# Kernel tuning notes

Measured on AMD Instinct MI355X. Metric: run time of the kernel, lower is better.

Reference implementation:

```python
import jax, jax.numpy as jnp
import numpy as np

N, F, H, CLS = 50000, 64, 128, 64   # nodes, node_features, second_features, num_classes
E, EL = 800000, 200000              # graph edges, decode (label) edges


def setup_inputs() -> dict:
    key = jax.random.key(0)
    ks = jax.random.split(key, 12)
    sc = lambda k, sh, fan: (jax.random.normal(k, sh, jnp.float32) / np.sqrt(fan)).astype(jnp.float32)
    return dict(
        x=jax.random.normal(ks[0], (N, F), jnp.float32),
        edge_index=jax.random.randint(ks[1], (2, E), 0, N),
        edge_label_index=jax.random.randint(ks[2], (2, EL), 0, N),
        hidden1=jnp.zeros((N, H), jnp.float32),   # H state of GCLSTM
        hidden2=jnp.zeros((N, H), jnp.float32),   # C state of GCLSTM
        # GCNConv params
        W_gcn=sc(ks[3], (F, F), F),
        b_gcn=jnp.zeros((F,), jnp.float32),
        # GCLSTM params, gates stacked along last axis in order (i, f, c, o)
        Wx=sc(ks[4], (F, 4 * H), F),      # input->gate weights W_i..W_o
        Th=sc(ks[5], (H, 4 * H), H),      # ChebConv(K=1) thetas on H (pure linear)
        b_gate=jnp.zeros((4 * H,), jnp.float32),  # b_i, b_f, b_c, b_o
        b_conv=jnp.zeros((4 * H,), jnp.float32),  # ChebConv biases
        w_c=sc(ks[6], (3, H), H),         # peephole w_c_i, w_c_f, w_c_o
        # output Linear
        W_lin=sc(ks[7], (H, CLS), H),
        b_lin=jnp.zeros((CLS,), jnp.float32),
    )


def _gcn(x, src, dst, W, b, n):
    """PyG GCNConv: add self-loops, symmetric D^-1/2 (A+I) D^-1/2 normalization."""
    xw = x @ W                                   # [N,F]
    loop = jnp.arange(n)
    src = jnp.concatenate([src, loop])
    dst = jnp.concatenate([dst, loop])
    deg = jax.ops.segment_sum(jnp.ones(src.shape, jnp.float32), dst, num_segments=n)
    dinv = jnp.where(deg > 0, jax.lax.rsqrt(deg), 0.0)
    norm = dinv[src] * dinv[dst]                 # [E+N]
    agg = jax.ops.segment_sum(norm[:, None] * xw[src], dst, num_segments=n)
    return agg + b


def reference(x, edge_index, edge_label_index, hidden1, hidden2,
              W_gcn, b_gcn, Wx, Th, b_gate, b_conv, w_c, W_lin, b_lin):
    n = x.shape[0]
    h = _gcn(x, edge_index[0], edge_index[1], W_gcn, b_gcn, n)   # GCNConv  [N,F]
    # GCLSTM, K=1: ChebConv on H degenerates to H @ Theta + b_conv
    g = (h @ Wx + b_gate) + (hidden1 @ Th + b_conv)              # [N,4H]
    gi, gf, gc, go = jnp.split(g, 4, axis=1)
    I = jax.nn.sigmoid(gi + w_c[0] * hidden2)
    Fg = jax.nn.sigmoid(gf + w_c[1] * hidden2)
    C = Fg * hidden2 + I * jnp.tanh(gc)
    O = jax.nn.sigmoid(go + w_c[2] * C)          # peephole on NEW cell state
    Hn = O * jnp.tanh(C)                         # [N,H]
    z = jax.nn.softmax(jax.nn.relu(Hn) @ W_lin + b_lin, axis=1)  # [N,CLS]
    # decode: dot product of endpoint embeddings
    r = jnp.sum(z[edge_label_index[0]] * z[edge_label_index[1]], axis=-1)  # [EL]
    # faithful to the original forward: returns input hidden1 and the NEW cell state
    return (r, hidden1, C)
```

## Files before the change

### kernel.cpp

```cpp
#include <hip/hip_runtime.h>
#include <math.h>

#define FDIM 64
#define HDIM 128
#define CLSD 64

#define NPART 8
#define MAXDEG 64

typedef unsigned short ushort_t;
typedef _Float16 hfrag __attribute__((ext_vector_type(8)));
typedef float f32x4 __attribute__((ext_vector_type(4)));

#define LOG2E 1.4426950408889634f

__device__ __forceinline__ float ex2(float x){ float r; asm("v_exp_f32 %0, %1" : "=v"(r) : "v"(x)); return r; }
__device__ __forceinline__ float rcp_(float x){ float r; asm("v_rcp_f32 %0, %1" : "=v"(r) : "v"(x)); return r; }
__device__ __forceinline__ float fsigmoid(float x){ return rcp_(1.0f + ex2(-LOG2E*x)); }
__device__ __forceinline__ float ftanh(float x){ return 1.0f - 2.0f*rcp_(1.0f + ex2(2.0f*LOG2E*x)); }

__device__ __forceinline__ ushort_t f2h(float f){
    _Float16 h = (_Float16)f;
    ushort_t u; __builtin_memcpy(&u, &h, 2); return u;
}
__device__ __forceinline__ float hflo(unsigned int u){
    ushort_t v = (ushort_t)u; _Float16 h; __builtin_memcpy(&h, &v, 2); return (float)h;
}
__device__ __forceinline__ float hfhi(unsigned int u){
    ushort_t v = (ushort_t)(u >> 16); _Float16 h; __builtin_memcpy(&h, &v, 2); return (float)h;
}
__device__ __forceinline__ unsigned int pk2h(float a, float b){
    return (unsigned int)f2h(a) | ((unsigned int)f2h(b) << 16);
}


__launch_bounds__(256)
__global__ void k_pre(const float* __restrict__ x,  const float* __restrict__ Wg,
                      const float* __restrict__ bg,
                      const float* __restrict__ Wx, const float* __restrict__ Th,
                      const float* __restrict__ Wl,
                      const float* __restrict__ bga, const float* __restrict__ bco,
                      const float* __restrict__ h1,
                      ushort_t* __restrict__ Bh, ushort_t* __restrict__ Lh,
                      float* __restrict__ bsum, int* __restrict__ cnt,
                      ushort_t* __restrict__ xh, ushort_t* __restrict__ Ab,
                      float* __restrict__ oh1, int N, int N2){
    int tid = blockIdx.x*256 + threadIdx.x;
    const int secW = 107008 + N;
    const int secX = secW + N*8;
    if (tid < 98304){
        int k = tid >> 9, col = tid & 511;
        float v;
        if (k < 64){
            float acc = 0.f;
            #pragma unroll 8
            for (int f = 0; f < 64; ++f) acc += Wg[k*64 + f]*Wx[f*512 + col];
            v = acc;
        } else {
            v = Th[(k-64)*512 + col];
        }
        int g = col >> 7, hc = col & 127;
        int w = hc >> 5, within = hc & 31;
        int c8 = g*2 + (within >> 4);
        int T = w*8 + c8;
        int s = k >> 5;
        int lane = ((k >> 3) & 3)*16 + (within & 15);
        int pos = ((T*6 + s)*64 + lane)*8 + (k & 7);
        Bh[pos] = f2h(v);
    } else if (tid < 106496){
        int i = tid - 98304;
        int k = i >> 6, col = i & 63;
        float v = Wl[k*64 + col];
        int ct = col >> 4;
        int s = k >> 5;
        int lane = ((k >> 3) & 3)*16 + (col & 15);
        int pos = ((ct*4 + s)*64 + lane)*8 + (k & 7);
        Lh[pos] = f2h(v);
    } else if (tid < 107008){
        int c = tid - 106496;
        float acc = bga[c] + bco[c];
        #pragma unroll 8
        for (int f = 0; f < 64; ++f) acc += bg[f]*Wx[f*512 + c];
        bsum[c] = acc;
    } else if (tid < secW){
        cnt[tid - 107008] = 0;
    } else if (tid < secX){
        int i = tid - secW;
        const float4* xp = (const float4*)(x + (size_t)i*8);
        float4 p0 = xp[0], p1 = xp[1];
        ((int4*)xh)[i] = make_int4((int)pk2h(p0.x,p0.y), (int)pk2h(p0.z,p0.w),
                                   (int)pk2h(p1.x,p1.y), (int)pk2h(p1.z,p1.w));
    } else {
        int i = tid - secX;
        if (i >= N2*16) return;
        int n = i >> 4, q = i & 15;
        int4 frag = make_int4(0,0,0,0);
        if (n < N){
            const float4* src = (const float4*)(h1 + (size_t)n*128 + q*8);
            float4 p0 = src[0], p1 = src[1];
            float4* dst = (float4*)(oh1 + (size_t)n*128 + q*8);
            dst[0] = p0; dst[1] = p1;
            frag = make_int4((int)pk2h(p0.x,p0.y), (int)pk2h(p0.z,p0.w),
                             (int)pk2h(p1.x,p1.y), (int)pk2h(p1.z,p1.w));
        }
        int s = 2 + (q >> 2);
        int lane = (q & 3)*16 + (n & 15);
        ((int4*)Ab)[((size_t)(n >> 4)*6 + s)*64 + lane] = frag;
    }
}

__launch_bounds__(256)
__global__ void k_fill(const int* __restrict__ ei, int* __restrict__ cnt,
                       int* __restrict__ ell, int E, int psz){
    int p   = blockIdx.x % NPART;
    int bi  = blockIdx.x / NPART;
    int bpp = gridDim.x / NPART;
    int chunk = (E + bpp - 1) / bpp;
    int beg = bi*chunk;
    int end = beg + chunk; if (end > E) end = E;
    int lo = p*psz, hi = lo + psz;
    for (int i = beg + threadIdx.x; i < end; i += 256){
        int d = ei[E + i];
        if (d >= lo && d < hi){
            int s = ei[i];
            int slot = atomicAdd(&cnt[d], 1);
            if (slot < MAXDEG) ell[(size_t)d*MAXDEG + slot] = s;
        }
    }
}

__launch_bounds__(256)
__global__ void k_dinv(const int* __restrict__ cnt, float* __restrict__ dinv, int N){
    int i = blockIdx.x*256 + threadIdx.x;
    if (i < N) dinv[i] = rsqrtf((float)cnt[i] + 1.0f);
}

__launch_bounds__(256)
__global__ void k_gather(const int* __restrict__ cnt, const int* __restrict__ ell,
                         const float* __restrict__ dinv, const ushort_t* __restrict__ xh,
                         ushort_t* __restrict__ Ab, int N, int N2){
    int tid = blockIdx.x*256 + threadIdx.x;
    int n = tid >> 3, q = tid & 7;
    if (n >= N2) return;
    int s_ = q >> 2;
    int lane = (q & 3)*16 + (n & 15);
    size_t fpos = ((size_t)(n >> 4)*6 + s_)*64 + lane;
    if (n >= N){
        ((int4*)Ab)[fpos] = make_int4(0,0,0,0);
        return;
    }
    int cn = cnt[n]; if (cn > MAXDEG) cn = MAXDEG;
    const int* row = ell + (size_t)n*MAXDEG;
    const int4* xv = (const int4*)xh;
    float a0=0.f,a1=0.f,a2=0.f,a3=0.f,a4=0.f,a5=0.f,a6=0.f,a7=0.f;
    int idx = 0;
    for (; idx + 4 <= cn; idx += 4){
        int s0 = row[idx], s1 = row[idx+1], s2 = row[idx+2], s3 = row[idx+3];
        float w0 = dinv[s0], w1 = dinv[s1], w2 = dinv[s2], w3 = dinv[s3];
        int4 u = xv[(size_t)s0*8 + q];
        int4 p = xv[(size_t)s1*8 + q];
        int4 v = xv[(size_t)s2*8 + q];
        int4 z = xv[(size_t)s3*8 + q];
        a0 += w0*hflo((unsigned)u.x) + w1*hflo((unsigned)p.x) + w2*hflo((unsigned)v.x) + w3*hflo((unsigned)z.x);
        a1 += w0*hfhi((unsigned)u.x) + w1*hfhi((unsigned)p.x) + w2*hfhi((unsigned)v.x) + w3*hfhi((unsigned)z.x);
        a2 += w0*hflo((unsigned)u.y) + w1*hflo((unsigned)p.y) + w2*hflo((unsigned)v.y) + w3*hflo((unsigned)z.y);
        a3 += w0*hfhi((unsigned)u.y) + w1*hfhi((unsigned)p.y) + w2*hfhi((unsigned)v.y) + w3*hfhi((unsigned)z.y);
        a4 += w0*hflo((unsigned)u.z) + w1*hflo((unsigned)p.z) + w2*hflo((unsigned)v.z) + w3*hflo((unsigned)z.z);
        a5 += w0*hfhi((unsigned)u.z) + w1*hfhi((unsigned)p.z) + w2*hfhi((unsigned)v.z) + w3*hfhi((unsigned)z.z);
        a6 += w0*hflo((unsigned)u.w) + w1*hflo((unsigned)p.w) + w2*hflo((unsigned)v.w) + w3*hflo((unsigned)z.w);
        a7 += w0*hfhi((unsigned)u.w) + w1*hfhi((unsigned)p.w) + w2*hfhi((unsigned)v.w) + w3*hfhi((unsigned)z.w);
    }
    for (; idx < cn; ++idx){
        int s0 = row[idx];
        float w0 = dinv[s0];
        int4 u = xv[(size_t)s0*8 + q];
        a0 += w0*hflo((unsigned)u.x); a1 += w0*hfhi((unsigned)u.x);
        a2 += w0*hflo((unsigned)u.y); a3 += w0*hfhi((unsigned)u.y);
        a4 += w0*hflo((unsigned)u.z); a5 += w0*hfhi((unsigned)u.z);
        a6 += w0*hflo((unsigned)u.w); a7 += w0*hfhi((unsigned)u.w);
    }
    float dn = dinv[n];
    int4 sv = xv[(size_t)n*8 + q];
    a0 = dn*(a0 + dn*hflo((unsigned)sv.x));
    a1 = dn*(a1 + dn*hfhi((unsigned)sv.x));
    a2 = dn*(a2 + dn*hflo((unsigned)sv.y));
    a3 = dn*(a3 + dn*hfhi((unsigned)sv.y));
    a4 = dn*(a4 + dn*hflo((unsigned)sv.z));
    a5 = dn*(a5 + dn*hfhi((unsigned)sv.z));
    a6 = dn*(a6 + dn*hflo((unsigned)sv.w));
    a7 = dn*(a7 + dn*hfhi((unsigned)sv.w));
    ((int4*)Ab)[fpos] = make_int4((int)pk2h(a0,a1), (int)pk2h(a2,a3),
                                  (int)pk2h(a4,a5), (int)pk2h(a6,a7));
}

__launch_bounds__(512)
__global__ void k_fused(const ushort_t* __restrict__ Ab, const float* __restrict__ h2,
                        const ushort_t* __restrict__ Bh, const ushort_t* __restrict__ Lh,
                        const float* __restrict__ bsum, const float* __restrict__ wc,
                        const float* __restrict__ blin,
                        float* __restrict__ outC, ushort_t* __restrict__ zb, int N)
{
    __shared__ __align__(16) char smem[33792];
    ushort_t* Hh   = (ushort_t*)smem;
    float*    Ltile = (float*)(smem + 16384);

    const int t    = threadIdx.x;
    const int w    = t >> 6;
    const int wm   = w >> 2;
    const int wn   = w & 3;
    const int lane = t & 63;
    const int nb   = blockIdx.x * 64;
    const size_t bt = (size_t)blockIdx.x * 4;

    f32x4 acc[2][8];
    #pragma unroll
    for (int mt = 0; mt < 2; ++mt)
        #pragma unroll
        for (int c8 = 0; c8 < 8; ++c8)
            acc[mt][c8] = (f32x4){0.f,0.f,0.f,0.f};

    const hfrag* AF  = (const hfrag*)Ab;
    const hfrag* BhF = (const hfrag*)Bh;

    #pragma unroll
    for (int s = 0; s < 6; ++s){
        hfrag a0 = AF[((bt + wm*2 + 0)*6 + s)*64 + lane];
        hfrag a1 = AF[((bt + wm*2 + 1)*6 + s)*64 + lane];
        #pragma unroll
        for (int c8 = 0; c8 < 8; ++c8){
            int T = wn*8 + c8;
            hfrag bh = BhF[(T*6 + s)*64 + lane];
            acc[0][c8] = __builtin_amdgcn_mfma_f32_16x16x32_f16(a0, bh, acc[0][c8], 0,0,0);
            acc[1][c8] = __builtin_amdgcn_mfma_f32_16x16x32_f16(a1, bh, acc[1][c8], 0,0,0);
        }
    }

    #pragma unroll
    for (int hc_t = 0; hc_t < 2; ++hc_t){
        int hc  = wn*32 + hc_t*16 + (lane & 15);
        float bi = bsum[hc],       bfv = bsum[128 + hc];
        float bc = bsum[256 + hc], bo  = bsum[384 + hc];
        float wci = wc[hc], wcf = wc[128 + hc], wco = wc[256 + hc];
        #pragma unroll
        for (int mt = 0; mt < 2; ++mt){
            #pragma unroll
            for (int rr = 0; rr < 4; ++rr){
                int row = wm*32 + mt*16 + ((lane >> 4) & 3)*4 + rr;
                int gr  = nb + row;
                float gi = acc[mt][0 + hc_t][rr] + bi;
                float gf = acc[mt][2 + hc_t][rr] + bfv;
                float gc = acc[mt][4 + hc_t][rr] + bc;
                float go = acc[mt][6 + hc_t][rr] + bo;
                float hv = (gr < N) ? h2[(size_t)gr*128 + hc] : 0.0f;
                float I  = fsigmoid(gi + wci*hv);
                float Fg = fsigmoid(gf + wcf*hv);
                float C  = Fg*hv + I*ftanh(gc);
                float O  = fsigmoid(go + wco*C);
                float hn = O*ftanh(C);
                if (gr < N) outC[(size_t)gr*128 + hc] = C;
                float hr = fmaxf(hn, 0.0f);
                int l2  = (row & 15) + (hc_t*2 + ((lane >> 3) & 1))*16;
                int pos = (((wm*2 + mt)*4 + wn)*64 + l2)*8 + (lane & 7);
                Hh[pos] = f2h(hr);
            }
        }
    }
    __syncthreads();

    const hfrag* HF  = (const hfrag*)Hh;
    const hfrag* LhF = (const hfrag*)Lh;
    f32x4 acc2[2];
    acc2[0] = (f32x4){0.f,0.f,0.f,0.f};
    acc2[1] = (f32x4){0.f,0.f,0.f,0.f};
    #pragma unroll
    for (int sp = 0; sp < 4; ++sp){
        hfrag a0 = HF[((wm*2+0)*4 + sp)*64 + lane];
        hfrag a1 = HF[((wm*2+1)*4 + sp)*64 + lane];
        hfrag bh = LhF[(wn*4 + sp)*64 + lane];
        acc2[0] = __builtin_amdgcn_mfma_f32_16x16x32_f16(a0, bh, acc2[0], 0,0,0);
        acc2[1] = __builtin_amdgcn_mfma_f32_16x16x32_f16(a1, bh, acc2[1], 0,0,0);
    }
    {
        int cls = wn*16 + (lane & 15);
        float bv = blin[cls];
        #pragma unroll
        for (int mtl = 0; mtl < 2; ++mtl){
            #pragma unroll
            for (int rr = 0; rr < 4; ++rr){
                int row = wm*32 + mtl*16 + ((lane >> 4) & 3)*4 + rr;
                Ltile[row*68 + cls] = acc2[mtl][rr] + bv;
            }
        }
    }
    __syncthreads();

    {
        int m = t >> 3, q = t & 7;
        const float4* Lr = (const float4*)&Ltile[m*68 + q*8];
        float4 v0 = Lr[0], v1 = Lr[1];
        float mx = fmaxf(fmaxf(fmaxf(v0.x,v0.y),fmaxf(v0.z,v0.w)),
                         fmaxf(fmaxf(v1.x,v1.y),fmaxf(v1.z,v1.w)));
        #pragma unroll
        for (int off2 = 1; off2 < 8; off2 <<= 1) mx = fmaxf(mx, __shfl_xor(mx, off2, 64));
        float e[8];
        e[0]=ex2(LOG2E*(v0.x-mx)); e[1]=ex2(LOG2E*(v0.y-mx));
        e[2]=ex2(LOG2E*(v0.z-mx)); e[3]=ex2(LOG2E*(v0.w-mx));
        e[4]=ex2(LOG2E*(v1.x-mx)); e[5]=ex2(LOG2E*(v1.y-mx));
        e[6]=ex2(LOG2E*(v1.z-mx)); e[7]=ex2(LOG2E*(v1.w-mx));
        float s8 = e[0]+e[1]+e[2]+e[3]+e[4]+e[5]+e[6]+e[7];
        #pragma unroll
        for (int off2 = 1; off2 < 8; off2 <<= 1) s8 += __shfl_xor(s8, off2, 64);
        float inv = rcp_(s8);
        if (nb + m < N){
            ((int4*)zb)[(size_t)(nb+m)*8 + q] =
                make_int4((int)pk2h(e[0]*inv, e[1]*inv), (int)pk2h(e[2]*inv, e[3]*inv),
                          (int)pk2h(e[4]*inv, e[5]*inv), (int)pk2h(e[6]*inv, e[7]*inv));
        }
    }
}

__launch_bounds__(256)
__global__ void k_dec(const int* __restrict__ eli, const ushort_t* __restrict__ zb,
                      float* __restrict__ r, int EL){
    int tid = blockIdx.x*256 + threadIdx.x;
    int e = tid >> 3, l = tid & 7;
    if (e >= EL) return;
    int s = eli[e], d = eli[EL + e];
    int4 a = ((const int4*)zb)[(size_t)s*8 + l];
    int4 b = ((const int4*)zb)[(size_t)d*8 + l];
    unsigned int ua[4] = {(unsigned)a.x,(unsigned)a.y,(unsigned)a.z,(unsigned)a.w};
    unsigned int ub[4] = {(unsigned)b.x,(unsigned)b.y,(unsigned)b.z,(unsigned)b.w};
    float p = 0.f;
    #pragma unroll
    for (int j = 0; j < 4; ++j){
        p += hflo(ua[j])*hflo(ub[j]) + hfhi(ua[j])*hfhi(ub[j]);
    }
    #pragma unroll
    for (int off = 1; off < 8; off <<= 1) p += __shfl_xor(p, off, 64);
    if (l == 0) r[e] = p;
}

extern "C" void kernel_launch(void* const* d_in, const int* in_sizes, int n_in,
                              void* d_out, int out_size, void* d_ws, size_t ws_size,
                              hipStream_t stream)
{
    const float* x   = (const float*)d_in[0];
    const int*   ei  = (const int*)  d_in[1];
    const int*   eli = (const int*)  d_in[2];
    const float* h1  = (const float*)d_in[3];
    const float* h2  = (const float*)d_in[4];
    const float* Wg  = (const float*)d_in[5];
    const float* bg  = (const float*)d_in[6];
    const float* Wx  = (const float*)d_in[7];
    const float* Th  = (const float*)d_in[8];
    const float* bga = (const float*)d_in[9];
    const float* bco = (const float*)d_in[10];
    const float* wc  = (const float*)d_in[11];
    const float* Wl  = (const float*)d_in[12];
    const float* bl  = (const float*)d_in[13];

    const int N  = in_sizes[0] / FDIM;
    const int E  = in_sizes[1] / 2;
    const int EL = in_sizes[2] / 2;
    const int N2 = (N + 63) & ~63;
    const int PSZ = (N + NPART - 1) / NPART;

    float* ws   = (float*)d_ws;
    ushort_t* xh = (ushort_t*)ws;
    ushort_t* Ab = xh + (size_t)N*64;
    ushort_t* zb = Ab + (size_t)N2*192;
    float* dinv = (float*)(zb + (size_t)N*64);
    int*   cnt  = (int*)(dinv + N);
    int*   ell  = cnt + N;
    size_t base = (size_t)((ell + (size_t)N*MAXDEG) - (int*)ws);
    base = (base + 3) & ~(size_t)3;
    ushort_t* Bh = (ushort_t*)(ws + base);
    ushort_t* Lh = Bh + 98304;
    float*  bsum = (float*)(Lh + 8192);

    float* out = (float*)d_out;
    float* r   = out;
    float* oh1 = out + EL;
    float* oC  = out + EL + (size_t)N*HDIM;

    const int preThreads = 107008 + N + N*8 + N2*16;
    const int epBlocks   = NPART * 256;
    k_pre   <<<(preThreads + 255)/256, 256, 0, stream>>>(x, Wg, bg, Wx, Th, Wl, bga, bco,
                                                         h1, Bh, Lh, bsum, cnt,
                                                         xh, Ab, oh1, N, N2);
    k_fill  <<<epBlocks, 256, 0, stream>>>(ei, cnt, ell, E, PSZ);
    k_dinv  <<<(N + 255)/256, 256, 0, stream>>>(cnt, dinv, N);
    k_gather<<<((size_t)N2*8 + 255)/256, 256, 0, stream>>>(cnt, ell, dinv, xh, Ab, N, N2);
    k_fused <<<N2/64, 512, 0, stream>>>(Ab, h2, Bh, Lh, bsum, wc, bl, oC, zb, N);
    k_dec   <<<(EL*8 + 255)/256, 256, 0, stream>>>(eli, zb, r, EL);
}
```

Baseline: 121.0 us.

## Merge edge fill into prep kernel, drop dinv pass, shrink fused tile

The edge-bucketing (ELL fill) is folded into the preprocessing kernel as extra blocks, and the degree counter is zeroed with an async memset. The separate dinv kernel is removed and gather computes rsqrt of the degree counts inline. The fused GEMM/LSTM/softmax kernel now uses 16-row tiles with 256 threads and less shared memory, giving more blocks for occupancy. The aim is fewer launches and better occupancy, at the cost of redundant rsqrt work and the B-weight fragments being reloaded by four times as many blocks.

```diff
diff --git a/kernel.cpp b/kernel.cpp
--- a/kernel.cpp
+++ b/kernel.cpp
@@ -40,14 +40,34 @@
                       const float* __restrict__ Wx, const float* __restrict__ Th,
                       const float* __restrict__ Wl,
                       const float* __restrict__ bga, const float* __restrict__ bco,
-                      const float* __restrict__ h1,
+                      const float* __restrict__ h1, const int* __restrict__ ei,
                       ushort_t* __restrict__ Bh, ushort_t* __restrict__ Lh,
                       float* __restrict__ bsum, int* __restrict__ cnt,
+                      int* __restrict__ ell,
                       ushort_t* __restrict__ xh, ushort_t* __restrict__ Ab,
-                      float* __restrict__ oh1, int N, int N2){
-    int tid = blockIdx.x*256 + threadIdx.x;
-    const int secW = 107008 + N;
-    const int secX = secW + N*8;
+                      float* __restrict__ oh1, int N, int N2, int E, int psz,
+                      int epBlocks){
+    int t = threadIdx.x;
+    if ((int)blockIdx.x < epBlocks){
+        int p   = blockIdx.x % NPART;
+        int bi  = blockIdx.x / NPART;
+        int bpp = epBlocks / NPART;
+        int chunk = (E + bpp - 1) / bpp;
+        int beg = bi*chunk;
+        int end = beg + chunk; if (end > E) end = E;
+        int lo = p*psz, hi = lo + psz;
+        for (int i = beg + t; i < end; i += 256){
+            int d = ei[E + i];
+            if (d >= lo && d < hi){
+                int s = ei[i];
+                int slot = atomicAdd(&cnt[d], 1);
+                if (slot < MAXDEG) ell[(size_t)d*MAXDEG + slot] = s;
+            }
+        }
+        return;
+    }
+    int tid = ((int)blockIdx.x - epBlocks)*256 + t;
+    const int secX = 107008 + N*8;
     if (tid < 98304){
         int k = tid >> 9, col = tid & 511;
         float v;
@@ -82,10 +102,8 @@
         #pragma unroll 8
         for (int f = 0; f < 64; ++f) acc += bg[f]*Wx[f*512 + c];
         bsum[c] = acc;
-    } else if (tid < secW){
-        cnt[tid - 107008] = 0;
     } else if (tid < secX){
-        int i = tid - secW;
+        int i = tid - 107008;
         const float4* xp = (const float4*)(x + (size_t)i*8);
         float4 p0 = xp[0], p1 = xp[1];
         ((int4*)xh)[i] = make_int4((int)pk2h(p0.x,p0.y), (int)pk2h(p0.z,p0.w),
@@ -110,34 +128,8 @@
 }
 
 __launch_bounds__(256)
-__global__ void k_fill(const int* __restrict__ ei, int* __restrict__ cnt,
-                       int* __restrict__ ell, int E, int psz){
-    int p   = blockIdx.x % NPART;
-    int bi  = blockIdx.x / NPART;
-    int bpp = gridDim.x / NPART;
-    int chunk = (E + bpp - 1) / bpp;
-    int beg = bi*chunk;
-    int end = beg + chunk; if (end > E) end = E;
-    int lo = p*psz, hi = lo + psz;
-    for (int i = beg + threadIdx.x; i < end; i += 256){
-        int d = ei[E + i];
-        if (d >= lo && d < hi){
-            int s = ei[i];
-            int slot = atomicAdd(&cnt[d], 1);
-            if (slot < MAXDEG) ell[(size_t)d*MAXDEG + slot] = s;
-        }
-    }
-}
-
-__launch_bounds__(256)
-__global__ void k_dinv(const int* __restrict__ cnt, float* __restrict__ dinv, int N){
-    int i = blockIdx.x*256 + threadIdx.x;
-    if (i < N) dinv[i] = rsqrtf((float)cnt[i] + 1.0f);
-}
-
-__launch_bounds__(256)
 __global__ void k_gather(const int* __restrict__ cnt, const int* __restrict__ ell,
-                         const float* __restrict__ dinv, const ushort_t* __restrict__ xh,
+                         const ushort_t* __restrict__ xh,
                          ushort_t* __restrict__ Ab, int N, int N2){
     int tid = blockIdx.x*256 + threadIdx.x;
     int n = tid >> 3, q = tid & 7;
@@ -156,7 +148,10 @@
     int idx = 0;
     for (; idx + 4 <= cn; idx += 4){
         int s0 = row[idx], s1 = row[idx+1], s2 = row[idx+2], s3 = row[idx+3];
-        float w0 = dinv[s0], w1 = dinv[s1], w2 = dinv[s2], w3 = dinv[s3];
+        float w0 = rsqrtf((float)cnt[s0] + 1.0f);
+        float w1 = rsqrtf((float)cnt[s1] + 1.0f);
+        float w2 = rsqrtf((float)cnt[s2] + 1.0f);
+        float w3 = rsqrtf((float)cnt[s3] + 1.0f);
         int4 u = xv[(size_t)s0*8 + q];
         int4 p = xv[(size_t)s1*8 + q];
         int4 v = xv[(size_t)s2*8 + q];
@@ -172,14 +167,14 @@
     }
     for (; idx < cn; ++idx){
         int s0 = row[idx];
-        float w0 = dinv[s0];
+        float w0 = rsqrtf((float)cnt[s0] + 1.0f);
         int4 u = xv[(size_t)s0*8 + q];
         a0 += w0*hflo((unsigned)u.x); a1 += w0*hfhi((unsigned)u.x);
         a2 += w0*hflo((unsigned)u.y); a3 += w0*hfhi((unsigned)u.y);
         a4 += w0*hflo((unsigned)u.z); a5 += w0*hfhi((unsigned)u.z);
         a6 += w0*hflo((unsigned)u.w); a7 += w0*hfhi((unsigned)u.w);
     }
-    float dn = dinv[n];
+    float dn = rsqrtf((float)cn + 1.0f);
     int4 sv = xv[(size_t)n*8 + q];
     a0 = dn*(a0 + dn*hflo((unsigned)sv.x));
     a1 = dn*(a1 + dn*hfhi((unsigned)sv.x));
@@ -193,128 +188,104 @@
                                   (int)pk2h(a4,a5), (int)pk2h(a6,a7));
 }
 
-__launch_bounds__(512)
+__launch_bounds__(256)
 __global__ void k_fused(const ushort_t* __restrict__ Ab, const float* __restrict__ h2,
                         const ushort_t* __restrict__ Bh, const ushort_t* __restrict__ Lh,
                         const float* __restrict__ bsum, const float* __restrict__ wc,
                         const float* __restrict__ blin,
                         float* __restrict__ outC, ushort_t* __restrict__ zb, int N)
 {
-    __shared__ __align__(16) char smem[33792];
+    __shared__ __align__(16) char smem[8448];
     ushort_t* Hh   = (ushort_t*)smem;
-    float*    Ltile = (float*)(smem + 16384);
+    float*    Ltile = (float*)(smem + 4096);
 
     const int t    = threadIdx.x;
     const int w    = t >> 6;
-    const int wm   = w >> 2;
-    const int wn   = w & 3;
     const int lane = t & 63;
-    const int nb   = blockIdx.x * 64;
-    const size_t bt = (size_t)blockIdx.x * 4;
-
-    f32x4 acc[2][8];
-    #pragma unroll
-    for (int mt = 0; mt < 2; ++mt)
-        #pragma unroll
-        for (int c8 = 0; c8 < 8; ++c8)
-            acc[mt][c8] = (f32x4){0.f,0.f,0.f,0.f};
+    const int nb   = blockIdx.x * 16;
+
+    f32x4 acc[8];
+    #pragma unroll
+    for (int c8 = 0; c8 < 8; ++c8) acc[c8] = (f32x4){0.f,0.f,0.f,0.f};
 
     const hfrag* AF  = (const hfrag*)Ab;
     const hfrag* BhF = (const hfrag*)Bh;
 
     #pragma unroll
     for (int s = 0; s < 6; ++s){
-        hfrag a0 = AF[((bt + wm*2 + 0)*6 + s)*64 + lane];
-        hfrag a1 = AF[((bt + wm*2 + 1)*6 + s)*64 + lane];
+        hfrag a0 = AF[((size_t)blockIdx.x*6 + s)*64 + lane];
         #pragma unroll
         for (int c8 = 0; c8 < 8; ++c8){
-            int T = wn*8 + c8;
+            int T = w*8 + c8;
             hfrag bh = BhF[(T*6 + s)*64 + lane];
-            acc[0][c8] = __builtin_amdgcn_mfma_f32_16x16x32_f16(a0, bh, acc[0][c8], 0,0,0);
-            acc[1][c8] = __builtin_amdgcn_mfma_f32_16x16x32_f16(a1, bh, acc[1][c8], 0,0,0);
+            acc[c8] = __builtin_amdgcn_mfma_f32_16x16x32_f16(a0, bh, acc[c8], 0,0,0);
         }
     }
 
     #pragma unroll
     for (int hc_t = 0; hc_t < 2; ++hc_t){
-        int hc  = wn*32 + hc_t*16 + (lane & 15);
+        int hc  = w*32 + hc_t*16 + (lane & 15);
         float bi = bsum[hc],       bfv = bsum[128 + hc];
         float bc = bsum[256 + hc], bo  = bsum[384 + hc];
         float wci = wc[hc], wcf = wc[128 + hc], wco = wc[256 + hc];
         #pragma unroll
-        for (int mt = 0; mt < 2; ++mt){
-            #pragma unroll
-            for (int rr = 0; rr < 4; ++rr){
-                int row = wm*32 + mt*16 + ((lane >> 4) & 3)*4 + rr;
-                int gr  = nb + row;
-                float gi = acc[mt][0 + hc_t][rr] + bi;
-                float gf = acc[mt][2 + hc_t][rr] + bfv;
-                float gc = acc[mt][4 + hc_t][rr] + bc;
-                float go = acc[mt][6 + hc_t][rr] + bo;
-                float hv = (gr < N) ? h2[(size_t)gr*128 + hc] : 0.0f;
-                float I  = fsigmoid(gi + wci*hv);
-                float Fg = fsigmoid(gf + wcf*hv);
-                float C  = Fg*hv + I*ftanh(gc);
-                float O  = fsigmoid(go + wco*C);
-                float hn = O*ftanh(C);
-                if (gr < N) outC[(size_t)gr*128 + hc] = C;
-                float hr = fmaxf(hn, 0.0f);
-                int l2  = (row & 15) + (hc_t*2 + ((lane >> 3) & 1))*16;
-                int pos = (((wm*2 + mt)*4 + wn)*64 + l2)*8 + (lane & 7);
-                Hh[pos] = f2h(hr);
-            }
+        for (int rr = 0; rr < 4; ++rr){
+            int row = ((lane >> 4) & 3)*4 + rr;
+            int gr  = nb + row;
+            float gi = acc[0 + hc_t][rr] + bi;
+            float gf = acc[2 + hc_t][rr] + bfv;
+            float gc = acc[4 + hc_t][rr] + bc;
+            float go = acc[6 + hc_t][rr] + bo;
+            float hv = (gr < N) ? h2[(size_t)gr*128 + hc] : 0.0f;
+            float I  = fsigmoid(gi + wci*hv);
+            float Fg = fsigmoid(gf + wcf*hv);
+            float C  = Fg*hv + I*ftanh(gc);
+            float O  = fsigmoid(go + wco*C);
+            float hn = O*ftanh(C);
+            if (gr < N) outC[(size_t)gr*128 + hc] = C;
+            float hr = fmaxf(hn, 0.0f);
+            int l2  = row + (hc_t*2 + ((lane >> 3) & 1))*16;
+            int pos = (w*64 + l2)*8 + (lane & 7);
+            Hh[pos] = f2h(hr);
         }
     }
     __syncthreads();
 
     const hfrag* HF  = (const hfrag*)Hh;
     const hfrag* LhF = (const hfrag*)Lh;
-    f32x4 acc2[2];
-    acc2[0] = (f32x4){0.f,0.f,0.f,0.f};
-    acc2[1] = (f32x4){0.f,0.f,0.f,0.f};
+    f32x4 acc2 = (f32x4){0.f,0.f,0.f,0.f};
     #pragma unroll
     for (int sp = 0; sp < 4; ++sp){
-        hfrag a0 = HF[((wm*2+0)*4 + sp)*64 + lane];
-        hfrag a1 = HF[((wm*2+1)*4 + sp)*64 + lane];
-        hfrag bh = LhF[(wn*4 + sp)*64 + lane];
-        acc2[0] = __builtin_amdgcn_mfma_f32_16x16x32_f16(a0, bh, acc2[0], 0,0,0);
-        acc2[1] = __builtin_amdgcn_mfma_f32_16x16x32_f16(a1, bh, acc2[1], 0,0,0);
+        hfrag a0 = HF[sp*64 + lane];
+        hfrag bh = LhF[(w*4 + sp)*64 + lane];
+        acc2 = __builtin_amdgcn_mfma_f32_16x16x32_f16(a0, bh, acc2, 0,0,0);
     }
     {
-        int cls = wn*16 + (lane & 15);
+        int cls = w*16 + (lane & 15);
         float bv = blin[cls];
         #pragma unroll
-        for (int mtl = 0; mtl < 2; ++mtl){
-            #pragma unroll
-            for (int rr = 0; rr < 4; ++rr){
-                int row = wm*32 + mtl*16 + ((lane >> 4) & 3)*4 + rr;
-                Ltile[row*68 + cls] = acc2[mtl][rr] + bv;
-            }
+        for (int rr = 0; rr < 4; ++rr){
+            int row = ((lane >> 4) & 3)*4 + rr;
+            Ltile[row*68 + cls] = acc2[rr] + bv;
         }
     }
     __syncthreads();
 
     {
-        int m = t >> 3, q = t & 7;
-        const float4* Lr = (const float4*)&Ltile[m*68 + q*8];
-        float4 v0 = Lr[0], v1 = Lr[1];
-        float mx = fmaxf(fmaxf(fmaxf(v0.x,v0.y),fmaxf(v0.z,v0.w)),
-                         fmaxf(fmaxf(v1.x,v1.y),fmaxf(v1.z,v1.w)));
-        #pragma unroll
-        for (int off2 = 1; off2 < 8; off2 <<= 1) mx = fmaxf(mx, __shfl_xor(mx, off2, 64));
-        float e[8];
-        e[0]=ex2(LOG2E*(v0.x-mx)); e[1]=ex2(LOG2E*(v0.y-mx));
-        e[2]=ex2(LOG2E*(v0.z-mx)); e[3]=ex2(LOG2E*(v0.w-mx));
-        e[4]=ex2(LOG2E*(v1.x-mx)); e[5]=ex2(LOG2E*(v1.y-mx));
-        e[6]=ex2(LOG2E*(v1.z-mx)); e[7]=ex2(LOG2E*(v1.w-mx));
-        float s8 = e[0]+e[1]+e[2]+e[3]+e[4]+e[5]+e[6]+e[7];
-        #pragma unroll
-        for (int off2 = 1; off2 < 8; off2 <<= 1) s8 += __shfl_xor(s8, off2, 64);
-        float inv = rcp_(s8);
+        int m = t >> 4, q4 = t & 15;
+        float4 v0 = *(const float4*)&Ltile[m*68 + q4*4];
+        float mx = fmaxf(fmaxf(v0.x,v0.y), fmaxf(v0.z,v0.w));
+        #pragma unroll
+        for (int off2 = 1; off2 < 16; off2 <<= 1) mx = fmaxf(mx, __shfl_xor(mx, off2, 64));
+        float e0 = ex2(LOG2E*(v0.x-mx)), e1 = ex2(LOG2E*(v0.y-mx));
+        float e2 = ex2(LOG2E*(v0.z-mx)), e3 = ex2(LOG2E*(v0.w-mx));
+        float s4 = e0+e1+e2+e3;
+        #pragma unroll
+        for (int off2 = 1; off2 < 16; off2 <<= 1) s4 += __shfl_xor(s4, off2, 64);
+        float inv = rcp_(s4);
         if (nb + m < N){
-            ((int4*)zb)[(size_t)(nb+m)*8 + q] =
-                make_int4((int)pk2h(e[0]*inv, e[1]*inv), (int)pk2h(e[2]*inv, e[3]*inv),
-                          (int)pk2h(e[4]*inv, e[5]*inv), (int)pk2h(e[6]*inv, e[7]*inv));
+            uint2 o; o.x = pk2h(e0*inv, e1*inv); o.y = pk2h(e2*inv, e3*inv);
+            ((uint2*)zb)[(size_t)(nb+m)*16 + q4] = o;
         }
     }
 }
@@ -369,8 +340,7 @@
     ushort_t* xh = (ushort_t*)ws;
     ushort_t* Ab = xh + (size_t)N*64;
     ushort_t* zb = Ab + (size_t)N2*192;
-    float* dinv = (float*)(zb + (size_t)N*64);
-    int*   cnt  = (int*)(dinv + N);
+    int*   cnt  = (int*)(zb + (size_t)N*64);
     int*   ell  = cnt + N;
     size_t base = (size_t)((ell + (size_t)N*MAXDEG) - (int*)ws);
     base = (base + 3) & ~(size_t)3;
@@ -383,14 +353,16 @@
     float* oh1 = out + EL;
     float* oC  = out + EL + (size_t)N*HDIM;
 
-    const int preThreads = 107008 + N + N*8 + N2*16;
     const int epBlocks   = NPART * 256;
-    k_pre   <<<(preThreads + 255)/256, 256, 0, stream>>>(x, Wg, bg, Wx, Th, Wl, bga, bco,
-                                                         h1, Bh, Lh, bsum, cnt,
-                                                         xh, Ab, oh1, N, N2);
-    k_fill  <<<epBlocks, 256, 0, stream>>>(ei, cnt, ell, E, PSZ);
-    k_dinv  <<<(N + 255)/256, 256, 0, stream>>>(cnt, dinv, N);
-    k_gather<<<((size_t)N2*8 + 255)/256, 256, 0, stream>>>(cnt, ell, dinv, xh, Ab, N, N2);
-    k_fused <<<N2/64, 512, 0, stream>>>(Ab, h2, Bh, Lh, bsum, wc, bl, oC, zb, N);
+    const int preThreads = 107008 + N*8 + N2*16;
+    const int preBlocks  = (preThreads + 255)/256;
+
+    hipMemsetAsync(cnt, 0, (size_t)N*sizeof(int), stream);
+    k_pre   <<<epBlocks + preBlocks, 256, 0, stream>>>(x, Wg, bg, Wx, Th, Wl, bga, bco,
+                                                       h1, ei, Bh, Lh, bsum, cnt, ell,
+                                                       xh, Ab, oh1, N, N2, E, PSZ,
+                                                       epBlocks);
+    k_gather<<<((size_t)N2*8 + 255)/256, 256, 0, stream>>>(cnt, ell, xh, Ab, N, N2);
+    k_fused <<<N2/16, 256, 0, stream>>>(Ab, h2, Bh, Lh, bsum, wc, bl, oC, zb, N);
     k_dec   <<<(EL*8 + 255)/256, 256, 0, stream>>>(eli, zb, r, EL);
 }
```

After: 122.8 us. Within noise of the previous version (+1.5%).
